# Optimization experiments

Measured on AMD Instinct MI355X. Metric: run time of the kernel, lower is better.

## Reference

```python
import jax, jax.numpy as jnp
import numpy as np

N_WAY = 5
MAX_PER_CLASS = 256
SIGMA_GRID = np.array([0.5, 1.0, 2.0, 4.0], dtype=np.float32)
NUM_NEG = 1
GAMMA = 0.1
HARD_POOL = 8
MEDIAN_K = 512
EPS = 1e-12
LAMBDA_MMD = 0.1


def _pairwise_sq(x, y=None):
    # squared euclidean distances between rows of x [n,d] and y [m,d]
    if y is None:
        y = x
    x2 = jnp.sum(x * x, axis=1, keepdims=True)
    y2 = jnp.sum(y * y, axis=1, keepdims=True).T
    return jnp.maximum(x2 + y2 - 2.0 * (x @ y.T), 0.0)


def _row_norm(x):
    return x / (jnp.linalg.norm(x, axis=1, keepdims=True) + EPS)


def _rbf_multi(d, sigmas):
    # multi-bandwidth RBF kernel sum: sum_s exp(-d / (2 s^2))
    return jnp.sum(jnp.exp(-d[None] / (2.0 * sigmas[:, None, None] ** 2)), axis=0)


def _mmd2(Da, Db, Dab, sigmas):
    # biased MMD^2 estimator (unbiased=False)
    m = (_rbf_multi(Da, sigmas).mean() + _rbf_multi(Db, sigmas).mean()
         - 2.0 * _rbf_multi(Dab, sigmas).mean())
    return jnp.maximum(m, 0.0)


def _median_sigmas(xa, xb):
    # median-heuristic bandwidth (no grad); concat has <= MEDIAN_K rows by construction
    z = jnp.concatenate([xa, xb], axis=0)
    d = _pairwise_sq(z)
    ds = jnp.sort(d.ravel())
    n = ds.shape[0]
    nz = jnp.sum(d <= 0)  # number of zero entries (diag + exact dups)
    idx = jnp.minimum(nz + (n - nz - 1) // 2, n - 1)  # lower median of positive entries
    med = jnp.take(ds, idx)
    base = jnp.where(nz >= n, jnp.asarray(1.0, z.dtype), jnp.sqrt(med + 1e-6))
    return jax.lax.stop_gradient(base) * jnp.asarray(SIGMA_GRID, z.dtype)


def _gather_indices(l_s, l_q):
    # host-side ragged per-class index extraction + deterministic subsample
    ls = np.asarray(l_s)
    lq = np.asarray(l_q)
    sup, ns, qry, nq = {}, {}, {}, {}
    for c in range(1, N_WAY + 1):
        idx = np.nonzero(ls[c - 1] == 1)[0]
        if idx.size >= 2:
            ns[c] = int(idx.size)
            if idx.size > MAX_PER_CLASS:
                rng = np.random.default_rng(1000 + c)
                idx = idx[rng.permutation(idx.size)[:MAX_PER_CLASS]]
            sup[c] = idx
        m, nn = np.nonzero(lq == c)
        if m.size >= 2:
            nq[c] = int(m.size)
            if m.size > MAX_PER_CLASS:
                rng = np.random.default_rng(2000 + c)
                pick = rng.permutation(m.size)[:MAX_PER_CLASS]
                m, nn = m[pick], nn[pick]
            qry[c] = (m, nn)
    return sup, ns, qry, nq


def _class_feats(f_s, f_q, sup, qry):
    # gather per-class rows and L2-normalize them
    fq = jnp.transpose(f_q, (0, 2, 1))  # [M_B, Nb, C]
    xas = {c: _row_norm(f_s[c - 1].T[idx]) for c, idx in sup.items()}
    xbs = {c: _row_norm(fq[m, nn]) for c, (m, nn) in qry.items()}
    return xas, xbs


def _select_picks(f_s, f_q, sup, qry):
    # hard-negative selection on concrete values (detached in the original)
    xas, xbs = _class_feats(f_s, f_q, sup, qry)
    picks = {}
    for c in sorted(set(xas) & set(xbs)):
        xb = xbs[c]
        Db = _pairwise_sq(xb)
        sig_pos = _median_sigmas(xas[c], xb)
        neg = [k for k in xas if k != c]
        if NUM_NEG == 0 or not neg:
            picks[c] = []
            continue
        scr = [(float(_mmd2(_pairwise_sq(xas[k]), Db, _pairwise_sq(xas[k], xb), sig_pos)), k) for k in neg]
        scr.sort(key=lambda t: t[0])
        pool = [k for _, k in scr[:max(HARD_POOL, NUM_NEG)]]
        ex = [(float(_mmd2(_pairwise_sq(xas[k]), Db, _pairwise_sq(xas[k], xb), _median_sigmas(xas[k], xb))), k) for k in pool]
        ex.sort(key=lambda t: t[0])
        picks[c] = [k for _, k in ex[:NUM_NEG]]
    return picks


def _loss(f_s, f_q, sup, ns, qry, nq, picks):
    xas, xbs = _class_feats(f_s, f_q, sup, qry)
    total = jnp.zeros((), f_s.dtype)
    valid_w = jnp.zeros((), f_s.dtype)
    for c in sorted(set(xas) & set(xbs)):
        xa, xb = xas[c], xbs[c]
        Db = _pairwise_sq(xb)
        sig_pos = _median_sigmas(xa, xb)
        mmd_pos = _mmd2(_pairwise_sq(xa), Db, _pairwise_sq(xa, xb), sig_pos)
        negs = []
        for k in picks.get(c, []):
            xk = xas[k]
            sig_k = _median_sigmas(xk, xb)
            negs.append(_mmd2(_pairwise_sq(xk), Db, _pairwise_sq(xk, xb), sig_k))
        if negs:
            mmd_neg = jnp.stack(negs).mean()
            loss_c = jax.nn.relu(mmd_pos - mmd_neg + GAMMA)
        else:
            loss_c = mmd_pos
        w = (ns[c] * nq[c]) ** 0.5  # class_weight='sqrt_ns_nq'
        total = total + w * loss_c
        valid_w = valid_w + w
    return LAMBDA_MMD * total / jnp.maximum(valid_w, EPS)


def setup_inputs() -> dict:
    key = jax.random.key(0)
    k1, k2, k3, k4 = jax.random.split(key, 4)
    return {
        "f_s": jax.random.normal(k1, (5, 256, 16384), jnp.float32),
        "l_s": jax.random.randint(k2, (5, 16384), 0, 2, jnp.int32),
        "f_q": jax.random.normal(k3, (5, 256, 65536), jnp.float32),
        "l_q": jax.random.randint(k4, (5, 65536), 0, 6, jnp.int32),
    }


def reference(f_s, l_s, f_q, l_q):
    sup, ns, qry, nq = _gather_indices(l_s, l_q)
    picks = _select_picks(f_s, f_q, sup, qry)
    return _loss(f_s, f_q, sup, ns, qry, nq, picks)
```

## Files before the change

### kernel.cpp

```cpp
#include <hip/hip_runtime.h>

struct U128 { unsigned long long hi, lo; };

__device__ __forceinline__ U128 u128_mul(U128 a, U128 b) {
  U128 r;
  r.lo = a.lo * b.lo;
  r.hi = __umul64hi(a.lo, b.lo) + a.hi * b.lo + a.lo * b.hi;
  return r;
}
__device__ __forceinline__ U128 u128_add(U128 a, U128 b) {
  U128 r; r.lo = a.lo + b.lo; r.hi = a.hi + b.hi + (r.lo < a.lo ? 1ull : 0ull); return r;
}

struct Pcg64 {
  U128 state, inc;
};

__device__ __forceinline__ void pcg_step(Pcg64* r) {
  const U128 M = {0x2360ed051fc65da4ull, 0x4385df649fccf645ull};
  r->state = u128_add(u128_mul(r->state, M), r->inc);
}
__device__ __forceinline__ unsigned long long pcg_next64(Pcg64* r) {
  pcg_step(r);
  unsigned int rot = (unsigned int)(r->state.hi >> 58);
  unsigned long long x = r->state.hi ^ r->state.lo;
  return (x >> rot) | (x << ((64u - rot) & 63u));
}

__device__ __forceinline__ unsigned int ss_hashmix(unsigned int v, unsigned int* hc) {
  v ^= *hc; *hc = *hc * 0x931e8875u; v *= *hc; v ^= v >> 16; return v;
}
__device__ __forceinline__ unsigned int ss_mix(unsigned int x, unsigned int y) {
  unsigned int r = x * 0xca01f9ddu ^ y * 0x4973f715u; r ^= r >> 16; return r;
}
__device__ void pcg_seed(Pcg64* rng, unsigned int seed) {
  unsigned int pool[4]; unsigned int hc = 0x43b0d7e5u;
  pool[0] = ss_hashmix(seed, &hc);
  for (int i = 1; i < 4; ++i) pool[i] = ss_hashmix(0u, &hc);
  for (int s = 0; s < 4; ++s)
    for (int d = 0; d < 4; ++d)
      if (s != d) pool[d] = ss_mix(pool[d], ss_hashmix(pool[s], &hc));
  unsigned int hc2 = 0x8b51f9ddu;
  unsigned long long w64[4];
  for (int i = 0; i < 4; ++i) {
    unsigned int lo = pool[(2*i) & 3];
    lo ^= hc2; hc2 *= 0x58f38dedu; lo *= hc2; lo ^= lo >> 16;
    unsigned int hi = pool[(2*i+1) & 3];
    hi ^= hc2; hc2 *= 0x58f38dedu; hi *= hc2; hi ^= hi >> 16;
    w64[i] = (unsigned long long)lo | ((unsigned long long)hi << 32);
  }
  U128 initstate = {w64[0], w64[1]};
  U128 initseq   = {w64[2], w64[3]};
  rng->inc.hi = (initseq.hi << 1) | (initseq.lo >> 63);
  rng->inc.lo = (initseq.lo << 1) | 1ull;
  rng->state.hi = 0; rng->state.lo = 0;
  pcg_step(rng);
  rng->state = u128_add(rng->state, initstate);
  pcg_step(rng);
}

__device__ void pcg_advance(Pcg64* r, unsigned long long delta) {
  U128 acc_mult = {0ull, 1ull}, acc_plus = {0ull, 0ull};
  U128 cur_mult = {0x2360ed051fc65da4ull, 0x4385df649fccf645ull};
  U128 cur_plus = r->inc;
  while (delta) {
    if (delta & 1ull) {
      acc_mult = u128_mul(acc_mult, cur_mult);
      acc_plus = u128_add(u128_mul(acc_plus, cur_mult), cur_plus);
    }
    U128 one = {0ull, 1ull};
    U128 cm1 = u128_add(cur_mult, one);
    cur_plus = u128_mul(cm1, cur_plus);
    cur_mult = u128_mul(cur_mult, cur_mult);
    delta >>= 1;
  }
  r->state = u128_add(u128_mul(r->state, acc_mult), acc_plus);
}

#define S_LEN   16384
#define Q_LEN   65536
#define Q_TOT   327680
#define DFEAT   256
#define MAXS    256
#define CAPS64  24576
#define CAPQ64  98304
#define TILE    4096
#define STILES  (S_LEN / TILE)
#define QTILES  (Q_TOT / TILE)
#define NBLK_C  (5 * STILES + 5 * QTILES)
#define MSHARDS 8
#define MPASSES 8


__constant__ int c_kshift[MPASSES] = {27, 23, 19, 15, 11, 7, 3, 0};

__global__ __launch_bounds__(256) void k_draws(unsigned int* __restrict__ draws) {
  int t = blockIdx.x; int cls = t % 5; int isq = t / 5;
  unsigned int seed = (unsigned)(1000 + isq * 1000 + cls + 1);
  unsigned long long cap64 = isq ? CAPQ64 : CAPS64;
  unsigned int* dst = draws + (isq ? (10ull * CAPS64 + (unsigned long long)cls * 2 * CAPQ64)
                                   : ((unsigned long long)cls * 2 * CAPS64));
  Pcg64 rng; pcg_seed(&rng, seed);
  int tid = threadIdx.x;
  unsigned long long C = cap64 / 256ull;
  unsigned long long k0 = (unsigned long long)tid * C;
  pcg_advance(&rng, k0);
  uint2* d2 = (uint2*)dst;
  for (unsigned long long m = 0; m < C; ++m) {
    unsigned long long o = pcg_next64(&rng);
    d2[k0 + m] = make_uint2((unsigned int)o, (unsigned int)(o >> 32));
  }
}

__global__ __launch_bounds__(256) void k_count(const int* __restrict__ ls,
                                               const int* __restrict__ lq,
                                               int* __restrict__ cnts) {
  int b = blockIdx.x;
  const int* src; int matchval;
  if (b < 5 * STILES) {
    int cls = b / STILES, tl = b % STILES;
    src = ls + cls * S_LEN + tl * TILE; matchval = 1;
  } else {
    int bb = b - 5 * STILES; int cls = bb / QTILES, tl = bb % QTILES;
    src = lq + tl * TILE; matchval = cls + 1;
  }
  int tid = threadIdx.x;
  int cnt = 0;
  for (int k = 0; k < TILE; k += 256) cnt += (src[k + tid] == matchval) ? 1 : 0;
  __shared__ int red[256];
  red[tid] = cnt; __syncthreads();
  for (int s = 128; s > 0; s >>= 1) { if (tid < s) red[tid] += red[tid + s]; __syncthreads(); }
  if (tid == 0) cnts[b] = red[0];
}

__global__ void k_scan(const int* __restrict__ cnts, int* __restrict__ offs,
                       int* __restrict__ meta) {
  int t = threadIdx.x;
  if (t < 5) {
    int base = 0;
    for (int k = 0; k < STILES; ++k) {
      offs[t * STILES + k] = base; base += cnts[t * STILES + k];
    }
    meta[t] = base;
    meta[10 + t] = base < MAXS ? base : MAXS;
  } else if (t < 10) {
    int c = t - 5; int base = 0;
    for (int k = 0; k < QTILES; ++k) {
      int idx = 5 * STILES + c * QTILES + k;
      offs[idx] = base; base += cnts[idx];
    }
    meta[5 + c] = base;
    meta[15 + c] = base < MAXS ? base : MAXS;
  }
}

__global__ __launch_bounds__(256) void k_write(const int* __restrict__ ls,
                                               const int* __restrict__ lq,
                                               const int* __restrict__ offs,
                                               int* __restrict__ sup_list,
                                               int* __restrict__ qry_list) {
  int b = blockIdx.x;
  const int* src; int matchval; int* out; int ibase;
  if (b < 5 * STILES) {
    int cls = b / STILES, tl = b % STILES;
    src = ls + cls * S_LEN + tl * TILE; matchval = 1;
    out = sup_list + cls * S_LEN; ibase = tl * TILE;
  } else {
    int bb = b - 5 * STILES; int cls = bb / QTILES, tl = bb % QTILES;
    src = lq + tl * TILE; matchval = cls + 1;
    out = qry_list + (size_t)cls * Q_TOT; ibase = tl * TILE;
  }
  int tid = threadIdx.x; int w = tid >> 6, lane = tid & 63;
  unsigned long long lmask = (1ull << lane) - 1ull;
  __shared__ int wcnt[4];
  int base = offs[b];
  for (int k = 0; k < TILE; k += 256) {
    int i = k + tid;
    bool p = (src[i] == matchval);
    unsigned long long m = __ballot(p);
    if (lane == 0) wcnt[w] = __popcll(m);
    __syncthreads();
    int prev = 0;
    #pragma unroll
    for (int ww = 0; ww < 4; ++ww) prev += (ww < w) ? wcnt[ww] : 0;
    int tot = wcnt[0] + wcnt[1] + wcnt[2] + wcnt[3];
    if (p) out[base + prev + __popcll(m & lmask)] = ibase + i;
    __syncthreads();
    base += tot;
  }
}

__device__ __forceinline__ bool consume_chunk(unsigned int v, int& i, int n, int lane,
                                              unsigned long long lmask,
                                              unsigned long long lbit,
                                              unsigned int* __restrict__ ring) {
  unsigned long long rej = 0ull, acc = 0ull;
  for (;;) {
    unsigned long long unc = ~(rej | acc);
    int rbelow = __popcll(rej & lmask);
    int ubelow = __popcll(unc & lmask);
    int il_min = i - lane + rbelow;
    int il_max = il_min + ubelow;
    bool unres = (unc & lbit) != 0ull;
    unsigned int mlo = 0xFFFFFFFFu >> __clz(il_min);
    unsigned int mhi = 0xFFFFFFFFu >> __clz(il_max);
    unsigned int w = v & mlo;
    bool def_rej, hard;
    if (mlo == mhi) {
      def_rej = w > (unsigned int)il_max;
      hard = !def_rej && (w > (unsigned int)il_min);
    } else if (ubelow == 0) {
      def_rej = w > (unsigned int)il_min;
      hard = false;
    } else {
      def_rej = false;
      hard = true;
    }
    def_rej = def_rej && unres;
    hard = hard && unres;
    unsigned long long nr = __ballot(def_rej);
    unsigned long long hd = __ballot(hard);
    rej |= nr;
    acc |= unc & ~nr & ~hd;
    if (!hd) break;
  }
  int rbelow = __popcll(rej & lmask);
  int il = i - lane + rbelow;
  int totAcc = 64 - __popcll(rej);
  if ((acc & lbit) && il >= MAXS) {
    int g = (n - 1) - il;
    ring[g & 4095] = v & (0xFFFFFFFFu >> __clz(il));
  }
  int needed = i - (MAXS - 1);
  if (totAcc >= needed) return true;
  i -= totAcc;
  return false;
}

__global__ __launch_bounds__(64) void k_consume(const int* __restrict__ meta,
                                                const unsigned int* __restrict__ draws,
                                                int* Jsup, int* Jqry) {
  __shared__ unsigned int ring[4096];
  int t = blockIdx.x; int cls = t % 5; int isq = t / 5;
  int n = meta[isq * 5 + cls];
  if (n <= MAXS) return;
  const unsigned int* d = draws + (isq ? (10ull * CAPS64 + (unsigned long long)cls * 2 * CAPQ64)
                                       : ((unsigned long long)cls * 2 * CAPS64));
  int* J = isq ? (Jqry + (size_t)cls * Q_TOT) : (Jsup + cls * S_LEN);
  int lane = threadIdx.x;
  unsigned long long lmask = (1ull << lane) - 1ull;
  unsigned long long lbit  = (1ull << lane);
  int i = n - 1;
  size_t p = 0;
  int flushed = 0;
  const int cap = n - MAXS;
  unsigned int v0 = d[lane],       v1 = d[64 + lane];
  unsigned int v2 = d[128 + lane], v3 = d[192 + lane];
  unsigned int v4 = d[256 + lane], v5 = d[320 + lane];
  unsigned int v6 = d[384 + lane], v7 = d[448 + lane];
  for (;;) {
    unsigned int nv0 = d[p + 512 + lane];
    unsigned int nv1 = d[p + 576 + lane];
    unsigned int nv2 = d[p + 640 + lane];
    unsigned int nv3 = d[p + 704 + lane];
    unsigned int nv4 = d[p + 768 + lane];
    unsigned int nv5 = d[p + 832 + lane];
    unsigned int nv6 = d[p + 896 + lane];
    unsigned int nv7 = d[p + 960 + lane];
    bool done;
    if      (consume_chunk(v0, i, n, lane, lmask, lbit, ring)) done = true;
    else if (consume_chunk(v1, i, n, lane, lmask, lbit, ring)) done = true;
    else if (consume_chunk(v2, i, n, lane, lmask, lbit, ring)) done = true;
    else if (consume_chunk(v3, i, n, lane, lmask, lbit, ring)) done = true;
    else if (consume_chunk(v4, i, n, lane, lmask, lbit, ring)) done = true;
    else if (consume_chunk(v5, i, n, lane, lmask, lbit, ring)) done = true;
    else if (consume_chunk(v6, i, n, lane, lmask, lbit, ring)) done = true;
    else if (consume_chunk(v7, i, n, lane, lmask, lbit, ring)) done = true;
    else done = false;
    if (done) break;
    int avail = (n - 1) - i; if (avail > cap) avail = cap;
    while (avail - flushed >= 2048) {
      #pragma unroll
      for (int k = 0; k < 32; ++k) {
        int g = flushed + k * 64 + lane;
        J[(n - 1) - g] = (int)ring[g & 4095];
      }
      flushed += 2048;
    }
    p += 512;
    v0 = nv0; v1 = nv1; v2 = nv2; v3 = nv3;
    v4 = nv4; v5 = nv5; v6 = nv6; v7 = nv7;
  }
  for (int g = flushed + lane; g < cap; g += 64)
    J[(n - 1) - g] = (int)ring[g & 4095];
}

__global__ __launch_bounds__(256) void k_hfill(const int* __restrict__ meta,
                                               const int* __restrict__ Jsup,
                                               const int* __restrict__ Jqry,
                                               unsigned int* __restrict__ Hsup,
                                               unsigned int* __restrict__ Hqry) {
  const int SB = 5 * (S_LEN / 256);
  int b = blockIdx.x;
  int cls, i; const int* J; unsigned int* H; int n;
  if (b < SB) {
    cls = b / (S_LEN / 256);
    i = (b % (S_LEN / 256)) * 256 + threadIdx.x;
    n = meta[cls];
    J = Jsup + cls * S_LEN; H = Hsup + cls * S_LEN;
  } else {
    b -= SB;
    cls = b / (Q_TOT / 256);
    i = (b % (Q_TOT / 256)) * 256 + threadIdx.x;
    n = meta[5 + cls];
    J = Jqry + (size_t)cls * Q_TOT; H = Hqry + (size_t)cls * Q_TOT;
  }
  if (i < MAXS || i >= n) return;
  int j = J[i];
  if (j != i) atomicMin(&H[j], (unsigned int)i);
}

__global__ __launch_bounds__(256) void k_chase(const int* __restrict__ meta,
                                               const int* __restrict__ sup_list,
                                               const int* __restrict__ qry_list,
                                               const unsigned int* __restrict__ Hsup,
                                               const unsigned int* __restrict__ Hqry,
                                               int* sel) {
  int t = blockIdx.x; int tid = threadIdx.x;
  int cls = t % 5; int isq = t / 5;
  int n = meta[isq * 5 + cls];
  const int* list; const unsigned int* H;
  if (!isq) { list = sup_list + cls * S_LEN; H = Hsup + cls * S_LEN; }
  else      { list = qry_list + (size_t)cls * Q_TOT; H = Hqry + (size_t)cls * Q_TOT; }
  int* s = sel + t * MAXS;
  if (n <= MAXS) { if (tid < n) s[tid] = list[tid]; return; }
  unsigned int v = (unsigned int)tid;
  unsigned int h = H[v];
  while (h != 0xFFFFFFFFu) { v = h; h = H[v]; }
  s[tid] = list[v];
}

__global__ __launch_bounds__(256) void k_gather(const float* __restrict__ f_s,
                                                const float* __restrict__ f_q,
                                                const int* __restrict__ meta,
                                                const int* __restrict__ sel,
                                                float* xa, float* xb) {
  int blk = blockIdx.x;
  int t = blk >> 3;
  int slab = blk & 7;
  int cls = t % 5; int isq = t / 5;
  int n = meta[10 + isq * 5 + cls];
  int tid = threadIdx.x;
  int row = slab * 32 + (tid >> 3);
  int dg = tid & 7;
  if (row >= n) return;
  int id = sel[t * MAXS + row];
  const float* src; size_t stride; float* dst;
  if (!isq) {
    src = f_s + (size_t)cls * DFEAT * S_LEN + id; stride = S_LEN;
    dst = xa + cls * (MAXS * DFEAT) + row * DFEAT;
  } else {
    int m = id >> 16; int nn = id & 0xFFFF;
    src = f_q + (size_t)m * DFEAT * Q_LEN + nn; stride = Q_LEN;
    dst = xb + cls * (MAXS * DFEAT) + row * DFEAT;
  }
  float v[32];
  #pragma unroll
  for (int dd = 0; dd < 32; ++dd)
    v[dd] = src[(size_t)(dg * 32 + dd) * stride];
  float ss = 0.f;
  #pragma unroll
  for (int dd = 0; dd < 32; ++dd) ss += v[dd] * v[dd];
  ss += __shfl_xor(ss, 1);
  ss += __shfl_xor(ss, 2);
  ss += __shfl_xor(ss, 4);
  float inv = 1.0f / (sqrtf(ss) + 1e-12f);
  #pragma unroll
  for (int dd = 0; dd < 32; ++dd) dst[dg * 32 + dd] = v[dd] * inv;
}

__global__ __launch_bounds__(256) void k_gram(const float* __restrict__ xa,
                                              const float* __restrict__ xb,
                                              float* Ga, float* Gb, float* Gab) {
  int b = blockIdx.x;
  int j = b >> 2; int tile = b & 3;
  int tr = (tile >> 1) * 128, tc = (tile & 1) * 128;
  const float *A, *B; float* G;
  if (j < 5)       { A = xa + j * 65536; B = A; G = Ga + j * 65536; }
  else if (j < 10) { int c = j - 5; A = xb + c * 65536; B = A; G = Gb + c * 65536; }
  else             { int p = j - 10; int k = p / 5, c = p % 5;
                     A = xa + k * 65536; B = xb + c * 65536; G = Gab + p * 65536; }
  __shared__ float As[128][33];
  __shared__ float Bs[128][33];
  int tid = threadIdx.x;
  int w = tid >> 6, lane = tid & 63;
  int wr = w >> 1, wc = w & 1;
  int lr = lane >> 3, lc = lane & 7;
  int orow = wr * 64 + lr * 8;
  int ocol = wc * 64 + lc * 8;
  float acc[8][8];
  #pragma unroll
  for (int r = 0; r < 8; ++r)
    #pragma unroll
    for (int s = 0; s < 8; ++s) acc[r][s] = 0.f;

  for (int k0 = 0; k0 < 256; k0 += 32) {
    #pragma unroll
    for (int e = 0; e < 4; ++e) {
      int idx = tid + e * 256;
      int row = idx >> 3;
      int c4  = idx & 7;
      float4 va = *(const float4*)(A + (size_t)(tr + row) * 256 + k0 + c4 * 4);
      As[row][c4 * 4 + 0] = va.x; As[row][c4 * 4 + 1] = va.y;
      As[row][c4 * 4 + 2] = va.z; As[row][c4 * 4 + 3] = va.w;
      float4 vb = *(const float4*)(B + (size_t)(tc + row) * 256 + k0 + c4 * 4);
      Bs[row][c4 * 4 + 0] = vb.x; Bs[row][c4 * 4 + 1] = vb.y;
      Bs[row][c4 * 4 + 2] = vb.z; Bs[row][c4 * 4 + 3] = vb.w;
    }
    __syncthreads();
    #pragma unroll 4
    for (int kk = 0; kk < 32; ++kk) {
      float a[8], bv[8];
      #pragma unroll
      for (int r = 0; r < 8; ++r) a[r] = As[orow + r][kk];
      #pragma unroll
      for (int s = 0; s < 8; ++s) bv[s] = Bs[ocol + s][kk];
      #pragma unroll
      for (int r = 0; r < 8; ++r)
        #pragma unroll
        for (int s = 0; s < 8; ++s) acc[r][s] += a[r] * bv[s];
    }
    __syncthreads();
  }
  #pragma unroll
  for (int r = 0; r < 8; ++r) {
    float* grow = G + (size_t)(tr + orow + r) * 256 + tc + ocol;
    *(float4*)(grow + 0) = make_float4(acc[r][0], acc[r][1], acc[r][2], acc[r][3]);
    *(float4*)(grow + 4) = make_float4(acc[r][4], acc[r][5], acc[r][6], acc[r][7]);
  }
}

__global__ __launch_bounds__(256) void k_diag(const float* __restrict__ Ga,
                                              const float* __restrict__ Gb,
                                              float* diagA, float* diagB) {
  int t = blockIdx.x; int i = threadIdx.x;
  if (t < 5) diagA[t * 256 + i] = Ga[t * 65536 + i * 257];
  else { int c = t - 5; diagB[c * 256 + i] = Gb[c * 65536 + i * 257]; }
}

__global__ __launch_bounds__(256) void k_conv(float* Ga, float* Gb, float* Gab,
                                              const float* __restrict__ diagA,
                                              const float* __restrict__ diagB) {
  int b = blockIdx.x; int j = b >> 3; int slab = b & 7; int tid = threadIdx.x;
  float* G; const float *dA, *dB;
  if (j < 5)       { G = Ga + j * 65536; dA = diagA + j * 256; dB = dA; }
  else if (j < 10) { int c = j - 5; G = Gb + c * 65536; dA = diagB + c * 256; dB = dA; }
  else             { int p = j - 10; int k = p / 5, c = p % 5;
                     G = Gab + p * 65536; dA = diagA + k * 256; dB = diagB + c * 256; }
  float db = dB[tid];
  for (int i = slab * 32; i < slab * 32 + 32; ++i) {
    float g = G[i * 256 + tid];
    float d = dA[i] + db - 2.0f * g;
    G[i * 256 + tid] = d > 0.f ? d : 0.f;
  }
}

__device__ __forceinline__ void med_select(const unsigned int* __restrict__ c,
                                           unsigned int lprev, unsigned int bprev,
                                           unsigned int r, int kprev,
                                           unsigned int* lo, unsigned int* base) {
  int j = 15;
  #pragma unroll
  for (int q = 14; q >= 0; --q)
    if (bprev + c[q] > r) j = q;
  *lo = lprev + ((unsigned int)j << kprev);
  *base = (j == 0) ? bprev : bprev + c[j - 1];
}

__global__ __launch_bounds__(256) void k_medpass(int t,
                                                 const int* __restrict__ meta,
                                                 const float* __restrict__ Da_all,
                                                 const float* __restrict__ Db_all,
                                                 const float* __restrict__ Dab_all,
                                                 unsigned int* __restrict__ bufAll,
                                                 unsigned int* __restrict__ loArr,
                                                 unsigned int* __restrict__ baseArr,
                                                 unsigned int* __restrict__ zcArr) {
  int b = blockIdx.x;
  int p = b / MSHARDS, sh = b % MSHARDS;
  int kcl = p / 5, ccl = p % 5;
  int tid = threadIdx.x;
  int nsf = meta[kcl], nqf = meta[5 + ccl];
  if (nsf < 2 || nqf < 2) return;
  int na = meta[10 + kcl], nb = meta[15 + ccl];
  const float4* A4 = (const float4*)(Da_all + kcl * 65536);
  const float4* B4 = (const float4*)(Db_all + ccl * 65536);
  const float4* C4 = (const float4*)(Dab_all + p * 65536);

  __shared__ unsigned int sh_lo[1], sh_base[1];
  __shared__ unsigned int wred[4][16];
  __shared__ unsigned int wzc[4];

  int ks = c_kshift[t];
  unsigned int N = (unsigned int)(na + nb) * (unsigned int)(na + nb);

  if (tid == 0) {
    unsigned int lo = 0, base = 0;
    if (t > 0) {
      unsigned int nz = zcArr[p];
      if (nz < N) {
        unsigned int r = nz + (N - nz - 1u) / 2u;
        unsigned int cprev[15];
        const unsigned int* cp = bufAll + ((size_t)(t - 1) * 25 + p) * 16;
        #pragma unroll
        for (int q = 0; q < 15; ++q) cprev[q] = cp[q];
        med_select(cprev, loArr[(t - 1) * 25 + p], baseArr[(t - 1) * 25 + p],
                   r, c_kshift[t - 1], &lo, &base);
      }
    }
    sh_lo[0] = lo; sh_base[0] = base;
    if (sh == 0) { loArr[t * 25 + p] = lo; baseArr[t * 25 + p] = base; }
  }
  __syncthreads();
  unsigned int lo = sh_lo[0];

  unsigned int cnt[15];
  #pragma unroll
  for (int j = 0; j < 15; ++j) cnt[j] = 0;
  unsigned int zc = 0;
  unsigned int span = 16u << ks;

  #define PROC_MAT(M4, nr, nc, W)                                             \
    for (int m = 0; m < 8; ++m) {                                             \
      int fidx = sh * 2048 + m * 256 + tid;                                   \
      float4 v = M4[fidx];                                                    \
      int row = fidx >> 6; int col0 = (fidx & 63) << 2;                       \
      unsigned int kb[4] = {__float_as_uint(v.x), __float_as_uint(v.y),       \
                            __float_as_uint(v.z), __float_as_uint(v.w)};      \
      _Pragma("unroll")                                                       \
      for (int cc = 0; cc < 4; ++cc) {                                        \
        bool valid = (row < (nr)) && (col0 + cc < (nc));                      \
        unsigned int key = kb[cc];                                            \
        if (t == 0) zc += (valid && key == 0u) ? (W) : 0u;                    \
        unsigned int d = key - lo;                                            \
        bool in = valid && (key >= lo) && (d < span);                         \
        _Pragma("unroll")                                                     \
        for (int j = 0; j < 15; ++j)                                          \
          cnt[j] += (in && d < ((unsigned int)(j + 1) << ks)) ? (W) : 0u;     \
      }                                                                       \
    }

  PROC_MAT(A4, na, na, 1u)
  PROC_MAT(B4, nb, nb, 1u)
  PROC_MAT(C4, na, nb, 2u)
  #undef PROC_MAT

  #pragma unroll
  for (int j = 0; j < 15; ++j)
    for (int o = 32; o > 0; o >>= 1) cnt[j] += __shfl_down(cnt[j], o);
  if (t == 0)
    for (int o = 32; o > 0; o >>= 1) zc += __shfl_down(zc, o);
  int w = tid >> 6, lane = tid & 63;
  if (lane == 0) {
    #pragma unroll
    for (int j = 0; j < 15; ++j) wred[w][j] = cnt[j];
    wzc[w] = zc;
  }
  __syncthreads();
  if (tid < 15) {
    unsigned int s = wred[0][tid] + wred[1][tid] + wred[2][tid] + wred[3][tid];
    atomicAdd(&bufAll[((size_t)t * 25 + p) * 16 + tid], s);
  }
  if (t == 0 && tid == 15) {
    unsigned int s = wzc[0] + wzc[1] + wzc[2] + wzc[3];
    atomicAdd(&zcArr[p], s);
  }
}

__global__ __launch_bounds__(256) void k_rbf(const int* __restrict__ meta,
                                             const float* __restrict__ Da_all,
                                             const float* __restrict__ Db_all,
                                             const float* __restrict__ Dab_all,
                                             const unsigned int* __restrict__ bufAll,
                                             const unsigned int* __restrict__ loArr,
                                             const unsigned int* __restrict__ baseArr,
                                             const unsigned int* __restrict__ zcArr,
                                             double* __restrict__ mmdsum) {
  int b = blockIdx.x;
  int p = b / MSHARDS, sh = b % MSHARDS;
  int kcl = p / 5, ccl = p % 5;
  int tid = threadIdx.x;
  int nsf = meta[kcl], nqf = meta[5 + ccl];
  if (nsf < 2 || nqf < 2) return;
  int na = meta[10 + kcl], nb = meta[15 + ccl];
  const float4* A4 = (const float4*)(Da_all + kcl * 65536);
  const float4* B4 = (const float4*)(Db_all + ccl * 65536);
  const float4* C4 = (const float4*)(Dab_all + p * 65536);

  unsigned int N = (unsigned int)(na + nb) * (unsigned int)(na + nb);
  unsigned int nz = zcArr[p];
  float base_s;
  if (nz >= N) base_s = 1.0f;
  else {
    unsigned int r = nz + (N - nz - 1u) / 2u;
    unsigned int cprev[15];
    const unsigned int* cp = bufAll + ((size_t)(MPASSES - 1) * 25 + p) * 16;
    #pragma unroll
    for (int q = 0; q < 15; ++q) cprev[q] = cp[q];
    unsigned int lo, bs;
    med_select(cprev, loArr[(MPASSES - 1) * 25 + p], baseArr[(MPASSES - 1) * 25 + p],
               r, 0, &lo, &bs);
    base_s = sqrtf(__uint_as_float(lo) + 1e-6f);
  }
  float g2 = base_s * base_s;
  float c0 = 1.0f / (2.0f * g2 * 0.25f);
  float c1 = 1.0f / (2.0f * g2 * 1.0f);
  float c2 = 1.0f / (2.0f * g2 * 4.0f);
  float c3 = 1.0f / (2.0f * g2 * 16.0f);

  double accA = 0.0, accB = 0.0, accAB = 0.0;
  #define RBF_MAT(M4, nr, nc, ACC)                                            \
    for (int m = 0; m < 8; ++m) {                                             \
      int fidx = sh * 2048 + m * 256 + tid;                                   \
      float4 v = M4[fidx];                                                    \
      int row = fidx >> 6; int col0 = (fidx & 63) << 2;                       \
      float vv[4] = {v.x, v.y, v.z, v.w};                                     \
      _Pragma("unroll")                                                       \
      for (int cc = 0; cc < 4; ++cc) {                                        \
        if ((row < (nr)) && (col0 + cc < (nc))) {                             \
          float d = vv[cc];                                                   \
          ACC += (double)(expf(-d * c0) + expf(-d * c1)                       \
                        + expf(-d * c2) + expf(-d * c3));                     \
        }                                                                     \
      }                                                                       \
    }
  RBF_MAT(A4, na, na, accA)
  RBF_MAT(B4, nb, nb, accB)
  RBF_MAT(C4, na, nb, accAB)
  #undef RBF_MAT

  for (int o = 32; o > 0; o >>= 1) {
    accA += __shfl_down(accA, o);
    accB += __shfl_down(accB, o);
    accAB += __shfl_down(accAB, o);
  }
  __shared__ double wsum[4][3];
  int w = tid >> 6, lane = tid & 63;
  if (lane == 0) { wsum[w][0] = accA; wsum[w][1] = accB; wsum[w][2] = accAB; }
  __syncthreads();
  if (tid == 0) {
    double sA = wsum[0][0] + wsum[1][0] + wsum[2][0] + wsum[3][0];
    double sB = wsum[0][1] + wsum[1][1] + wsum[2][1] + wsum[3][1];
    double sC = wsum[0][2] + wsum[1][2] + wsum[2][2] + wsum[3][2];
    atomicAdd(&mmdsum[p * 3 + 0], sA);
    atomicAdd(&mmdsum[p * 3 + 1], sB);
    atomicAdd(&mmdsum[p * 3 + 2], sC);
  }
}

__global__ void k_final(const int* __restrict__ meta, const double* __restrict__ mmdsum,
                        float* out) {
  if (threadIdx.x != 0 || blockIdx.x != 0) return;
  double total = 0.0, vw = 0.0;
  for (int c = 0; c < 5; ++c) {
    int nsf = meta[c], nqf = meta[5 + c];
    if (nsf < 2 || nqf < 2) continue;
    int nbq = meta[15 + c];
    double mm[5];
    for (int k = 0; k < 5; ++k) {
      if (meta[k] < 2) { mm[k] = 0.0; continue; }
      int naa = meta[10 + k];
      int pp = k * 5 + c;
      double meanA  = mmdsum[pp * 3 + 0] / ((double)naa * (double)naa);
      double meanB  = mmdsum[pp * 3 + 1] / ((double)nbq * (double)nbq);
      double meanAB = mmdsum[pp * 3 + 2] / ((double)naa * (double)nbq);
      double m = meanA + meanB - 2.0 * meanAB;
      mm[k] = m > 0.0 ? m : 0.0;
    }
    double pos = mm[c];
    bool any = false; double best = 0.0;
    for (int k = 0; k < 5; ++k) {
      if (k == c || meta[k] < 2) continue;
      if (!any || mm[k] < best) { best = mm[k]; any = true; }
    }
    double lc = any ? fmax(pos - best + 0.1, 0.0) : pos;
    double w = sqrt((double)nsf * (double)nqf);
    total += w * lc; vw += w;
  }
  out[0] = (float)(0.1 * total / fmax(vw, 1e-12));
}

extern "C" void kernel_launch(void* const* d_in, const int* in_sizes, int n_in,
                              void* d_out, int out_size, void* d_ws, size_t ws_size,
                              hipStream_t stream) {
  const float* f_s = (const float*)d_in[0];
  const int*   l_s = (const int*)d_in[1];
  const float* f_q = (const float*)d_in[2];
  const int*   l_q = (const int*)d_in[3];
  float* out = (float*)d_out;
  char* ws = (char*)d_ws;

  size_t off = 0;
  auto take = [&](size_t bytes) -> void* {
    void* p = ws + off;
    off = (off + bytes + 255) & ~(size_t)255;
    return p;
  };
  int*   meta     = (int*)take(32 * 4);
  int*   cnts     = (int*)take(NBLK_C * 4);
  int*   offs     = (int*)take(NBLK_C * 4);
  int*   sup_list = (int*)take((size_t)5 * S_LEN * 4);
  int*   qry_list = (int*)take((size_t)5 * Q_TOT * 4);
  int*   Jsup     = (int*)take((size_t)5 * S_LEN * 4);
  int*   Jqry     = (int*)take((size_t)5 * Q_TOT * 4);
  unsigned int* draws = (unsigned int*)take((10ull * CAPS64 + 10ull * CAPQ64) * 4);
  int*   sel      = (int*)take((size_t)10 * MAXS * 4);
  float* xa       = (float*)take((size_t)5 * 65536 * 4);
  float* xb       = (float*)take((size_t)5 * 65536 * 4);
  float* Ga       = (float*)take((size_t)5 * 65536 * 4);
  float* Gb       = (float*)take((size_t)5 * 65536 * 4);
  float* Gab      = (float*)take((size_t)25 * 65536 * 4);
  float* diagA    = (float*)take((size_t)5 * 256 * 4);
  float* diagB    = (float*)take((size_t)5 * 256 * 4);
  unsigned int* bufAll  = (unsigned int*)take((size_t)MPASSES * 25 * 16 * 4);
  unsigned int* loArr   = (unsigned int*)take((size_t)MPASSES * 25 * 4);
  unsigned int* baseArr = (unsigned int*)take((size_t)MPASSES * 25 * 4);
  unsigned int* zcArr   = (unsigned int*)take(25 * 4);
  double* mmdsum  = (double*)take(25 * 3 * 8);
  if (off > ws_size) return;

  unsigned int* Hsup = draws;
  unsigned int* Hqry = draws + (size_t)5 * S_LEN;
  size_t hbytes = ((size_t)5 * S_LEN + (size_t)5 * Q_TOT) * 4;

  k_draws<<<10, 256, 0, stream>>>(draws);
  k_count<<<NBLK_C, 256, 0, stream>>>(l_s, l_q, cnts);
  k_scan<<<1, 64, 0, stream>>>(cnts, offs, meta);
  k_write<<<NBLK_C, 256, 0, stream>>>(l_s, l_q, offs, sup_list, qry_list);
  k_consume<<<10, 64, 0, stream>>>(meta, draws, Jsup, Jqry);
  hipMemsetAsync(Hsup, 0xFF, hbytes, stream);
  {
    int nblk = 5 * (S_LEN / 256) + 5 * (Q_TOT / 256);
    k_hfill<<<nblk, 256, 0, stream>>>(meta, Jsup, Jqry, Hsup, Hqry);
  }
  k_chase<<<10, 256, 0, stream>>>(meta, sup_list, qry_list, Hsup, Hqry, sel);
  k_gather<<<80, 256, 0, stream>>>(f_s, f_q, meta, sel, xa, xb);
  k_gram<<<140, 256, 0, stream>>>(xa, xb, Ga, Gb, Gab);
  k_diag<<<10, 256, 0, stream>>>(Ga, Gb, diagA, diagB);
  k_conv<<<280, 256, 0, stream>>>(Ga, Gb, Gab, diagA, diagB);

  hipMemsetAsync(bufAll, 0, (size_t)MPASSES * 25 * 16 * 4, stream);
  hipMemsetAsync(zcArr, 0, 25 * 4, stream);
  hipMemsetAsync(mmdsum, 0, 25 * 3 * 8, stream);
  for (int t = 0; t < MPASSES; ++t)
    k_medpass<<<25 * MSHARDS, 256, 0, stream>>>(t, meta, Ga, Gb, Gab,
                                                bufAll, loArr, baseArr, zcArr);
  k_rbf<<<25 * MSHARDS, 256, 0, stream>>>(meta, Ga, Gb, Gab,
                                          bufAll, loArr, baseArr, zcArr, mmdsum);
  k_final<<<1, 64, 0, stream>>>(meta, mmdsum, out);
}
```

Measured before the change: 761.7 us.

## Fuse chase into gather, diag into gram, and recompute distances on the fly

Folds the hash-chain chase into the gather kernel, extracts the Gram diagonal inside the gram kernel, and drops the separate distance-conversion pass. The median passes and the RBF kernel now rebuild squared distances from the Gram entries and the diagonal norms each time they read them. The three small memsets become one contiguous memset. This removes four launches, one full read-write sweep over the Gram matrices and several memset calls, at the cost of a little extra arithmetic in every median pass.

```diff
diff --git a/kernel.cpp b/kernel.cpp
--- a/kernel.cpp
+++ b/kernel.cpp
@@ -320,41 +320,33 @@
   if (j != i) atomicMin(&H[j], (unsigned int)i);
 }
 
-__global__ __launch_bounds__(256) void k_chase(const int* __restrict__ meta,
-                                               const int* __restrict__ sup_list,
-                                               const int* __restrict__ qry_list,
-                                               const unsigned int* __restrict__ Hsup,
-                                               const unsigned int* __restrict__ Hqry,
-                                               int* sel) {
-  int t = blockIdx.x; int tid = threadIdx.x;
-  int cls = t % 5; int isq = t / 5;
-  int n = meta[isq * 5 + cls];
-  const int* list; const unsigned int* H;
-  if (!isq) { list = sup_list + cls * S_LEN; H = Hsup + cls * S_LEN; }
-  else      { list = qry_list + (size_t)cls * Q_TOT; H = Hqry + (size_t)cls * Q_TOT; }
-  int* s = sel + t * MAXS;
-  if (n <= MAXS) { if (tid < n) s[tid] = list[tid]; return; }
-  unsigned int v = (unsigned int)tid;
-  unsigned int h = H[v];
-  while (h != 0xFFFFFFFFu) { v = h; h = H[v]; }
-  s[tid] = list[v];
-}
-
 __global__ __launch_bounds__(256) void k_gather(const float* __restrict__ f_s,
                                                 const float* __restrict__ f_q,
                                                 const int* __restrict__ meta,
-                                                const int* __restrict__ sel,
+                                                const int* __restrict__ sup_list,
+                                                const int* __restrict__ qry_list,
+                                                const unsigned int* __restrict__ Hsup,
+                                                const unsigned int* __restrict__ Hqry,
                                                 float* xa, float* xb) {
   int blk = blockIdx.x;
   int t = blk >> 3;
   int slab = blk & 7;
   int cls = t % 5; int isq = t / 5;
+  int nfull = meta[isq * 5 + cls];
   int n = meta[10 + isq * 5 + cls];
   int tid = threadIdx.x;
   int row = slab * 32 + (tid >> 3);
   int dg = tid & 7;
   if (row >= n) return;
-  int id = sel[t * MAXS + row];
+  const int* list; const unsigned int* H;
+  if (!isq) { list = sup_list + cls * S_LEN; H = Hsup + cls * S_LEN; }
+  else      { list = qry_list + (size_t)cls * Q_TOT; H = Hqry + (size_t)cls * Q_TOT; }
+  unsigned int v = (unsigned int)row;
+  if (nfull > MAXS) {
+    unsigned int h = H[v];
+    while (h != 0xFFFFFFFFu) { v = h; h = H[v]; }
+  }
+  int id = list[v];
   const float* src; size_t stride; float* dst;
   if (!isq) {
     src = f_s + (size_t)cls * DFEAT * S_LEN + id; stride = S_LEN;
@@ -364,24 +356,25 @@
     src = f_q + (size_t)m * DFEAT * Q_LEN + nn; stride = Q_LEN;
     dst = xb + cls * (MAXS * DFEAT) + row * DFEAT;
   }
-  float v[32];
+  float vv[32];
   #pragma unroll
   for (int dd = 0; dd < 32; ++dd)
-    v[dd] = src[(size_t)(dg * 32 + dd) * stride];
+    vv[dd] = src[(size_t)(dg * 32 + dd) * stride];
   float ss = 0.f;
   #pragma unroll
-  for (int dd = 0; dd < 32; ++dd) ss += v[dd] * v[dd];
+  for (int dd = 0; dd < 32; ++dd) ss += vv[dd] * vv[dd];
   ss += __shfl_xor(ss, 1);
   ss += __shfl_xor(ss, 2);
   ss += __shfl_xor(ss, 4);
   float inv = 1.0f / (sqrtf(ss) + 1e-12f);
   #pragma unroll
-  for (int dd = 0; dd < 32; ++dd) dst[dg * 32 + dd] = v[dd] * inv;
+  for (int dd = 0; dd < 32; ++dd) dst[dg * 32 + dd] = vv[dd] * inv;
 }
 
 __global__ __launch_bounds__(256) void k_gram(const float* __restrict__ xa,
                                               const float* __restrict__ xb,
-                                              float* Ga, float* Gb, float* Gab) {
+                                              float* Ga, float* Gb, float* Gab,
+                                              float* diagA, float* diagB) {
   int b = blockIdx.x;
   int j = b >> 2; int tile = b & 3;
   int tr = (tile >> 1) * 128, tc = (tile & 1) * 128;
@@ -438,30 +431,18 @@
     *(float4*)(grow + 0) = make_float4(acc[r][0], acc[r][1], acc[r][2], acc[r][3]);
     *(float4*)(grow + 4) = make_float4(acc[r][4], acc[r][5], acc[r][6], acc[r][7]);
   }
-}
-
-__global__ __launch_bounds__(256) void k_diag(const float* __restrict__ Ga,
-                                              const float* __restrict__ Gb,
-                                              float* diagA, float* diagB) {
-  int t = blockIdx.x; int i = threadIdx.x;
-  if (t < 5) diagA[t * 256 + i] = Ga[t * 65536 + i * 257];
-  else { int c = t - 5; diagB[c * 256 + i] = Gb[c * 65536 + i * 257]; }
-}
-
-__global__ __launch_bounds__(256) void k_conv(float* Ga, float* Gb, float* Gab,
-                                              const float* __restrict__ diagA,
-                                              const float* __restrict__ diagB) {
-  int b = blockIdx.x; int j = b >> 3; int slab = b & 7; int tid = threadIdx.x;
-  float* G; const float *dA, *dB;
-  if (j < 5)       { G = Ga + j * 65536; dA = diagA + j * 256; dB = dA; }
-  else if (j < 10) { int c = j - 5; G = Gb + c * 65536; dA = diagB + c * 256; dB = dA; }
-  else             { int p = j - 10; int k = p / 5, c = p % 5;
-                     G = Gab + p * 65536; dA = diagA + k * 256; dB = diagB + c * 256; }
-  float db = dB[tid];
-  for (int i = slab * 32; i < slab * 32 + 32; ++i) {
-    float g = G[i * 256 + tid];
-    float d = dA[i] + db - 2.0f * g;
-    G[i * 256 + tid] = d > 0.f ? d : 0.f;
+  if (j < 10 && tr == tc) {
+    #pragma unroll
+    for (int r = 0; r < 8; ++r)
+      #pragma unroll
+      for (int s = 0; s < 8; ++s) {
+        int gr = orow + r, gc = ocol + s;
+        if (gr == gc) {
+          int gi = tr + gr;
+          if (j < 5) diagA[j * 256 + gi] = acc[r][s];
+          else       diagB[(j - 5) * 256 + gi] = acc[r][s];
+        }
+      }
   }
 }
 
@@ -479,9 +460,11 @@
 
 __global__ __launch_bounds__(256) void k_medpass(int t,
                                                  const int* __restrict__ meta,
-                                                 const float* __restrict__ Da_all,
-                                                 const float* __restrict__ Db_all,
-                                                 const float* __restrict__ Dab_all,
+                                                 const float* __restrict__ Ga_all,
+                                                 const float* __restrict__ Gb_all,
+                                                 const float* __restrict__ Gab_all,
+                                                 const float* __restrict__ diagA,
+                                                 const float* __restrict__ diagB,
                                                  unsigned int* __restrict__ bufAll,
                                                  unsigned int* __restrict__ loArr,
                                                  unsigned int* __restrict__ baseArr,
@@ -493,9 +476,11 @@
   int nsf = meta[kcl], nqf = meta[5 + ccl];
   if (nsf < 2 || nqf < 2) return;
   int na = meta[10 + kcl], nb = meta[15 + ccl];
-  const float4* A4 = (const float4*)(Da_all + kcl * 65536);
-  const float4* B4 = (const float4*)(Db_all + ccl * 65536);
-  const float4* C4 = (const float4*)(Dab_all + p * 65536);
+  const float4* A4 = (const float4*)(Ga_all + kcl * 65536);
+  const float4* B4 = (const float4*)(Gb_all + ccl * 65536);
+  const float4* C4 = (const float4*)(Gab_all + p * 65536);
+  const float* dAv = diagA + kcl * 256;
+  const float* dBv = diagB + ccl * 256;
 
   __shared__ unsigned int sh_lo[1], sh_base[1];
   __shared__ unsigned int wred[4][16];
@@ -530,13 +515,19 @@
   unsigned int zc = 0;
   unsigned int span = 16u << ks;
 
-  #define PROC_MAT(M4, nr, nc, W)                                             \
+  #define PROC_MAT(M4, DR, DC, nr, nc, W)                                     \
     for (int m = 0; m < 8; ++m) {                                             \
       int fidx = sh * 2048 + m * 256 + tid;                                   \
-      float4 v = M4[fidx];                                                    \
+      float4 g4 = M4[fidx];                                                   \
       int row = fidx >> 6; int col0 = (fidx & 63) << 2;                       \
-      unsigned int kb[4] = {__float_as_uint(v.x), __float_as_uint(v.y),       \
-                            __float_as_uint(v.z), __float_as_uint(v.w)};      \
+      float dr = DR[row];                                                     \
+      float4 dc4 = *(const float4*)((DC) + col0);                             \
+      float r0_ = dr + dc4.x - 2.0f * g4.x; float e0 = r0_ > 0.f ? r0_ : 0.f; \
+      float r1_ = dr + dc4.y - 2.0f * g4.y; float e1 = r1_ > 0.f ? r1_ : 0.f; \
+      float r2_ = dr + dc4.z - 2.0f * g4.z; float e2 = r2_ > 0.f ? r2_ : 0.f; \
+      float r3_ = dr + dc4.w - 2.0f * g4.w; float e3 = r3_ > 0.f ? r3_ : 0.f; \
+      unsigned int kb[4] = {__float_as_uint(e0), __float_as_uint(e1),         \
+                            __float_as_uint(e2), __float_as_uint(e3)};        \
       _Pragma("unroll")                                                       \
       for (int cc = 0; cc < 4; ++cc) {                                        \
         bool valid = (row < (nr)) && (col0 + cc < (nc));                      \
@@ -550,9 +541,9 @@
       }                                                                       \
     }
 
-  PROC_MAT(A4, na, na, 1u)
-  PROC_MAT(B4, nb, nb, 1u)
-  PROC_MAT(C4, na, nb, 2u)
+  PROC_MAT(A4, dAv, dAv, na, na, 1u)
+  PROC_MAT(B4, dBv, dBv, nb, nb, 1u)
+  PROC_MAT(C4, dAv, dBv, na, nb, 2u)
   #undef PROC_MAT
 
   #pragma unroll
@@ -578,9 +569,11 @@
 }
 
 __global__ __launch_bounds__(256) void k_rbf(const int* __restrict__ meta,
-                                             const float* __restrict__ Da_all,
-                                             const float* __restrict__ Db_all,
-                                             const float* __restrict__ Dab_all,
+                                             const float* __restrict__ Ga_all,
+                                             const float* __restrict__ Gb_all,
+                                             const float* __restrict__ Gab_all,
+                                             const float* __restrict__ diagA,
+                                             const float* __restrict__ diagB,
                                              const unsigned int* __restrict__ bufAll,
                                              const unsigned int* __restrict__ loArr,
                                              const unsigned int* __restrict__ baseArr,
@@ -593,9 +586,11 @@
   int nsf = meta[kcl], nqf = meta[5 + ccl];
   if (nsf < 2 || nqf < 2) return;
   int na = meta[10 + kcl], nb = meta[15 + ccl];
-  const float4* A4 = (const float4*)(Da_all + kcl * 65536);
-  const float4* B4 = (const float4*)(Db_all + ccl * 65536);
-  const float4* C4 = (const float4*)(Dab_all + p * 65536);
+  const float4* A4 = (const float4*)(Ga_all + kcl * 65536);
+  const float4* B4 = (const float4*)(Gb_all + ccl * 65536);
+  const float4* C4 = (const float4*)(Gab_all + p * 65536);
+  const float* dAv = diagA + kcl * 256;
+  const float* dBv = diagB + ccl * 256;
 
   unsigned int N = (unsigned int)(na + nb) * (unsigned int)(na + nb);
   unsigned int nz = zcArr[p];
@@ -619,24 +614,27 @@
   float c3 = 1.0f / (2.0f * g2 * 16.0f);
 
   double accA = 0.0, accB = 0.0, accAB = 0.0;
-  #define RBF_MAT(M4, nr, nc, ACC)                                            \
+  #define RBF_MAT(M4, DR, DC, nr, nc, ACC)                                    \
     for (int m = 0; m < 8; ++m) {                                             \
       int fidx = sh * 2048 + m * 256 + tid;                                   \
-      float4 v = M4[fidx];                                                    \
+      float4 g4 = M4[fidx];                                                   \
       int row = fidx >> 6; int col0 = (fidx & 63) << 2;                       \
-      float vv[4] = {v.x, v.y, v.z, v.w};                                     \
+      float dr = DR[row];                                                     \
+      float4 dc4 = *(const float4*)((DC) + col0);                             \
+      float rw[4] = {dr + dc4.x - 2.0f * g4.x, dr + dc4.y - 2.0f * g4.y,      \
+                     dr + dc4.z - 2.0f * g4.z, dr + dc4.w - 2.0f * g4.w};     \
       _Pragma("unroll")                                                       \
       for (int cc = 0; cc < 4; ++cc) {                                        \
         if ((row < (nr)) && (col0 + cc < (nc))) {                             \
-          float d = vv[cc];                                                   \
+          float d = rw[cc] > 0.f ? rw[cc] : 0.f;                              \
           ACC += (double)(expf(-d * c0) + expf(-d * c1)                       \
                         + expf(-d * c2) + expf(-d * c3));                     \
         }                                                                     \
       }                                                                       \
     }
-  RBF_MAT(A4, na, na, accA)
-  RBF_MAT(B4, nb, nb, accB)
-  RBF_MAT(C4, na, nb, accAB)
+  RBF_MAT(A4, dAv, dAv, na, na, accA)
+  RBF_MAT(B4, dBv, dBv, nb, nb, accB)
+  RBF_MAT(C4, dAv, dBv, na, nb, accAB)
   #undef RBF_MAT
 
   for (int o = 32; o > 0; o >>= 1) {
@@ -714,7 +712,6 @@
   int*   Jsup     = (int*)take((size_t)5 * S_LEN * 4);
   int*   Jqry     = (int*)take((size_t)5 * Q_TOT * 4);
   unsigned int* draws = (unsigned int*)take((10ull * CAPS64 + 10ull * CAPQ64) * 4);
-  int*   sel      = (int*)take((size_t)10 * MAXS * 4);
   float* xa       = (float*)take((size_t)5 * 65536 * 4);
   float* xb       = (float*)take((size_t)5 * 65536 * 4);
   float* Ga       = (float*)take((size_t)5 * 65536 * 4);
@@ -722,11 +719,13 @@
   float* Gab      = (float*)take((size_t)25 * 65536 * 4);
   float* diagA    = (float*)take((size_t)5 * 256 * 4);
   float* diagB    = (float*)take((size_t)5 * 256 * 4);
+  size_t zero0 = off;
   unsigned int* bufAll  = (unsigned int*)take((size_t)MPASSES * 25 * 16 * 4);
   unsigned int* loArr   = (unsigned int*)take((size_t)MPASSES * 25 * 4);
   unsigned int* baseArr = (unsigned int*)take((size_t)MPASSES * 25 * 4);
   unsigned int* zcArr   = (unsigned int*)take(25 * 4);
   double* mmdsum  = (double*)take(25 * 3 * 8);
+  size_t zero1 = off;
   if (off > ws_size) return;
 
   unsigned int* Hsup = draws;
@@ -743,19 +742,15 @@
     int nblk = 5 * (S_LEN / 256) + 5 * (Q_TOT / 256);
     k_hfill<<<nblk, 256, 0, stream>>>(meta, Jsup, Jqry, Hsup, Hqry);
   }
-  k_chase<<<10, 256, 0, stream>>>(meta, sup_list, qry_list, Hsup, Hqry, sel);
-  k_gather<<<80, 256, 0, stream>>>(f_s, f_q, meta, sel, xa, xb);
-  k_gram<<<140, 256, 0, stream>>>(xa, xb, Ga, Gb, Gab);
-  k_diag<<<10, 256, 0, stream>>>(Ga, Gb, diagA, diagB);
-  k_conv<<<280, 256, 0, stream>>>(Ga, Gb, Gab, diagA, diagB);
-
-  hipMemsetAsync(bufAll, 0, (size_t)MPASSES * 25 * 16 * 4, stream);
-  hipMemsetAsync(zcArr, 0, 25 * 4, stream);
-  hipMemsetAsync(mmdsum, 0, 25 * 3 * 8, stream);
+  k_gather<<<80, 256, 0, stream>>>(f_s, f_q, meta, sup_list, qry_list,
+                                   Hsup, Hqry, xa, xb);
+  k_gram<<<140, 256, 0, stream>>>(xa, xb, Ga, Gb, Gab, diagA, diagB);
+
+  hipMemsetAsync(ws + zero0, 0, zero1 - zero0, stream);
   for (int t = 0; t < MPASSES; ++t)
-    k_medpass<<<25 * MSHARDS, 256, 0, stream>>>(t, meta, Ga, Gb, Gab,
+    k_medpass<<<25 * MSHARDS, 256, 0, stream>>>(t, meta, Ga, Gb, Gab, diagA, diagB,
                                                 bufAll, loArr, baseArr, zcArr);
-  k_rbf<<<25 * MSHARDS, 256, 0, stream>>>(meta, Ga, Gb, Gab,
+  k_rbf<<<25 * MSHARDS, 256, 0, stream>>>(meta, Ga, Gb, Gab, diagA, diagB,
                                           bufAll, loArr, baseArr, zcArr, mmdsum);
   k_final<<<1, 64, 0, stream>>>(meta, mmdsum, out);
 }
```

Result: no change. 772.6 us (+1.4%).
